# Performance work log

Hardware: AMD Instinct MI355X
Metric: run time of the kernel (lower is better)

Reference implementation:

```python
import math
import jax, jax.numpy as jnp
import numpy as np

EPS = 1e-7
MAX_TANH_ARG = 1.0 - 1e-5

def _norm(x):
    return jnp.sqrt(jnp.sum(x * x, axis=-1, keepdims=True)).clip(EPS)

def logmap0(x):  # Poincare ball, c=1
    n = _norm(x)
    return jnp.arctanh(jnp.clip(n, EPS, MAX_TANH_ARG)) * x / n

def expmap0(v):
    n = _norm(v)
    return jnp.tanh(n) * v / n

def mobius_add(x, y):
    x2 = jnp.sum(x * x, -1, keepdims=True)
    y2 = jnp.sum(y * y, -1, keepdims=True)
    xy = jnp.sum(x * y, -1, keepdims=True)
    num = (1 + 2 * xy + y2) * x + (1 - x2) * y
    den = (1 + 2 * xy + x2 * y2).clip(EPS)
    return num / den

def plin(x, w, b):  # PoincareLinear: tangent-space affine map
    return expmap0(logmap0(x) @ w + b)

def layer_norm(x, eps=1e-6):  # elementwise_affine=False
    m = x.mean(-1, keepdims=True)
    v = ((x - m) ** 2).mean(-1, keepdims=True)
    return (x - m) / jnp.sqrt(v + eps)

def _beta(a, b):
    return math.exp(math.lgamma(a) + math.lgamma(b) - math.lgamma(a + b))

D, H, FF = 1024, 16, 4096
HD = D // H
BETA_N = _beta(D / 2, 0.5)   # beta(n/2, 1/2) for full dim
BETA_H = _beta(HD / 2, 0.5)  # beta(ni/2, 1/2) for head dim


def setup_inputs() -> dict:
    key = jax.random.key(0)
    ks = jax.random.split(key, 20)
    B, S = 4, 1024
    x = expmap0(0.02 * jax.random.normal(ks[0], (B, S, D), jnp.float32))
    t_emb = jax.random.normal(ks[1], (B, 1, D), jnp.float32)
    g = lambda k, sh: 0.02 * jax.random.normal(k, sh, jnp.float32)
    return {
        'x': x, 't_emb': t_emb,
        'w_q': g(ks[2], (D, D)), 'b_q': jnp.zeros((D,), jnp.float32),
        'w_k': g(ks[3], (D, D)), 'b_k': jnp.zeros((D,), jnp.float32),
        'w_v': g(ks[4], (D, D)), 'b_v': jnp.zeros((D,), jnp.float32),
        'w_o': g(ks[5], (D, D)), 'b_o': jnp.zeros((D,), jnp.float32),
        'w_f1': g(ks[6], (D, FF)), 'b_f1': jnp.zeros((FF,), jnp.float32),
        'w_f2': g(ks[7], (FF, D)), 'b_f2': jnp.zeros((D,), jnp.float32),
        'w_ada': g(ks[8], (D, 6 * D)), 'b_ada': jnp.zeros((6 * D,), jnp.float32),
    }


def _to_heads(p):
    # beta-split: logmap0, split per head, scale by beta_ni/beta_n, expmap0
    B, S, _ = p.shape
    t = logmap0(p).reshape(B, S, H, HD) * (BETA_H / BETA_N)
    return expmap0(jnp.transpose(t, (0, 2, 1, 3)))  # [B,H,S,HD]


def _from_heads(ph):
    # beta-concat: logmap0 per head, scale by beta_n/beta_ni, concat, expmap0
    B, _, S, _ = ph.shape
    t = logmap0(ph) * (BETA_N / BETA_H)
    t = jnp.transpose(t, (0, 2, 1, 3)).reshape(B, S, D)
    return expmap0(t)


def reference(x, t_emb, w_q, b_q, w_k, b_k, w_v, b_v, w_o, b_o,
              w_f1, b_f1, w_f2, b_f2, w_ada, b_ada):
    ada = t_emb @ w_ada + b_ada  # [B,1,6D]
    sh_msa, sc_msa, g_msa, sh_mlp, sc_mlp, g_mlp = jnp.split(ada, 6, axis=-1)

    # --- attention block ---
    residual = x
    xn = layer_norm(logmap0(x))
    xm = expmap0(xn * (1 + sc_msa) + sh_msa)

    q = _to_heads(plin(xm, w_q, b_q))
    k = _to_heads(plin(xm, w_k, b_k))
    v = _to_heads(plin(xm, w_v, b_v))

    qt, kt, vt = logmap0(q), logmap0(k), logmap0(v)
    scores = jnp.einsum('bhqd,bhkd->bhqk', qt, kt) / math.sqrt(HD)
    attn = jax.nn.softmax(scores, axis=-1)
    out_h = expmap0(jnp.einsum('bhqk,bhkd->bhqd', attn, vt))  # [B,H,S,HD]

    attn_out = plin(_from_heads(out_h), w_o, b_o)
    attn_t = g_msa * logmap0(attn_out)
    x = mobius_add(residual, expmap0(attn_t))

    # --- FFN block ---
    residual = x
    xn = layer_norm(logmap0(x))
    xm = expmap0(xn * (1 + sc_mlp) + sh_mlp)
    ff = plin(plin(xm, w_f1, b_f1), w_f2, b_f2)
    ff_t = g_mlp * logmap0(ff)
    return mobius_add(residual, expmap0(ff_t))
```

## Files before the change

kernel.cpp:

```cpp
#include <hip/hip_runtime.h>
#include <cmath>


constexpr int kD  = 1024;
constexpr int kH  = 16;
constexpr int kHD = 64;
constexpr int kFF = 4096;
constexpr int kB  = 4;
constexpr int kS  = 1024;
constexpr int kN  = kB * kS;

#define EPSF 1e-7f
#define MTAF (1.0f - 1e-5f)
#define LOG2E 1.4426950408889634f

typedef unsigned int uint32;
typedef unsigned short ushort16;
typedef __attribute__((ext_vector_type(8))) short short8x;
typedef __attribute__((ext_vector_type(4))) float floatx4;

__device__ __forceinline__ ushort16 f2b(float f) {
  union { float f; uint32 u; } x; x.f = f;
  uint32 r = x.u + 0x7fffu + ((x.u >> 16) & 1u);
  return (ushort16)(r >> 16);
}
__device__ __forceinline__ float b2f(ushort16 u) {
  union { uint32 u; float f; } x; x.u = ((uint32)u) << 16;
  return x.f;
}
__device__ __forceinline__ void load_b4(const ushort16* p, float v[4]) {
  uint2 u = *(const uint2*)p;
  v[0] = b2f((ushort16)(u.x & 0xffff)); v[1] = b2f((ushort16)(u.x >> 16));
  v[2] = b2f((ushort16)(u.y & 0xffff)); v[3] = b2f((ushort16)(u.y >> 16));
}
__device__ __forceinline__ void store_b4(ushort16* p, const float v[4]) {
  uint2 u;
  u.x = (uint32)f2b(v[0]) | ((uint32)f2b(v[1]) << 16);
  u.y = (uint32)f2b(v[2]) | ((uint32)f2b(v[3]) << 16);
  *(uint2*)p = u;
}

__device__ __forceinline__ float atanh_clipped(float n) {
  float c = fminf(n, MTAF);
  return 0.5f * logf((1.0f + c) / (1.0f - c));
}
__device__ __forceinline__ float logmap0_scale(float nraw) {
  float n = fmaxf(nraw, EPSF);
  return atanh_clipped(n) / n;
}
__device__ __forceinline__ float expmap0_scale(float nraw) {
  float n = fmaxf(nraw, EPSF);
  return tanhf(n) / n;
}
__device__ __forceinline__ float roundtrip_scale(float nraw) {
  float nu = fmaxf(nraw, EPSF);
  float se = tanhf(nu) / nu;
  float nb = fmaxf(se * nraw, EPSF);
  float sl = atanh_clipped(nb) / nb;
  return sl * se;
}

__device__ __forceinline__ float blockReduceSum256(float v, float* s4) {
#pragma unroll
  for (int o = 32; o > 0; o >>= 1) v += __shfl_xor(v, o);
  int wave = threadIdx.x >> 6;
  if ((threadIdx.x & 63) == 0) s4[wave] = v;
  __syncthreads();
  float r = s4[0] + s4[1] + s4[2] + s4[3];
  __syncthreads();
  return r;
}
__device__ __forceinline__ float redSum16(float v) {
#pragma unroll
  for (int o = 8; o > 0; o >>= 1) v += __shfl_xor(v, o);
  return v;
}

__device__ __forceinline__ void async16(const void* g, void* l) {
  __builtin_amdgcn_global_load_lds(
      (const __attribute__((address_space(1))) uint32*)g,
      (__attribute__((address_space(3))) uint32*)l, 16, 0, 0);
}

__device__ __forceinline__ void transpose_tile(const float* __restrict__ src,
                                               ushort16* __restrict__ dst,
                                               int K, int N, int n0, int k0) {
  __shared__ float T[64][65];
  int tid = threadIdx.x;
#pragma unroll
  for (int p = 0; p < 4; ++p) {
    int idx = p * 1024 + tid * 4;
    int r = idx >> 6, c = idx & 63;
    float4 t = *(const float4*)&src[(size_t)(k0 + r) * N + n0 + c];
    T[r][c] = t.x; T[r][c + 1] = t.y; T[r][c + 2] = t.z; T[r][c + 3] = t.w;
  }
  __syncthreads();
#pragma unroll
  for (int p = 0; p < 4; ++p) {
    int idx = p * 1024 + tid * 4;
    int r = idx >> 6, c = idx & 63;
    float v[4] = {T[c][r], T[c + 1][r], T[c + 2][r], T[c + 3][r]};
    store_b4(&dst[(size_t)(n0 + r) * K + k0 + c], v);
  }
}
__global__ __launch_bounds__(256) void k_transpose_bf16(const float* __restrict__ src,
                                                        ushort16* __restrict__ dst,
                                                        int K, int N) {
  transpose_tile(src, dst, K, N, blockIdx.x * 64, blockIdx.y * 64);
}
__global__ __launch_bounds__(256) void k_transpose4(
    const float* __restrict__ s0, const float* __restrict__ s1,
    const float* __restrict__ s2, const float* __restrict__ s3,
    ushort16* __restrict__ d0, ushort16* __restrict__ d1,
    ushort16* __restrict__ d2, ushort16* __restrict__ d3) {
  const float* src = (blockIdx.z == 0) ? s0 : (blockIdx.z == 1) ? s1
                    : (blockIdx.z == 2) ? s2 : s3;
  ushort16* dst = (blockIdx.z == 0) ? d0 : (blockIdx.z == 1) ? d1
                 : (blockIdx.z == 2) ? d2 : d3;
  transpose_tile(src, dst, kD, kD, blockIdx.x * 64, blockIdx.y * 64);
}

__global__ __launch_bounds__(256) void k_ada(const float* __restrict__ t_emb,
                                             const float* __restrict__ w_ada,
                                             const float* __restrict__ b_ada,
                                             float* __restrict__ ada) {
  __shared__ float te[kD];
  __shared__ float part[4][64];
  int b = blockIdx.y;
  int tid = threadIdx.x;
  {
    float4 t = *(const float4*)&t_emb[b * kD + tid * 4];
    te[tid * 4] = t.x; te[tid * 4 + 1] = t.y; te[tid * 4 + 2] = t.z; te[tid * 4 + 3] = t.w;
  }
  __syncthreads();
  int c = tid & 63, kc = tid >> 6;
  int col = blockIdx.x * 64 + c;
  float acc = 0.f;
#pragma unroll 8
  for (int k = kc * 256; k < kc * 256 + 256; ++k)
    acc += te[k] * w_ada[(size_t)k * (6 * kD) + col];
  part[kc][c] = acc;
  __syncthreads();
  if (tid < 64)
    ada[b * 6 * kD + blockIdx.x * 64 + tid] =
        part[0][tid] + part[1][tid] + part[2][tid] + part[3][tid] +
        b_ada[blockIdx.x * 64 + tid];
}

__global__ __launch_bounds__(256) void k_prenorm(const float* __restrict__ x,
                                                 const float* __restrict__ ada,
                                                 int sh_off, int sc_off,
                                                 ushort16* __restrict__ out) {
  __shared__ float sred[4];
  int tok = blockIdx.x;
  int b = tok >> 10;
  int d4 = threadIdx.x * 4;
  float xv[4];
  *(float4*)xv = *(const float4*)&x[(size_t)tok * kD + d4];
  float ss = xv[0] * xv[0] + xv[1] * xv[1] + xv[2] * xv[2] + xv[3] * xv[3];
  ss = blockReduceSum256(ss, sred);
  float sl = logmap0_scale(sqrtf(ss));
  float sum = 0.f;
#pragma unroll
  for (int i = 0; i < 4; ++i) { xv[i] *= sl; sum += xv[i]; }
  sum = blockReduceSum256(sum, sred);
  float mean = sum * (1.0f / kD);
  float vs = 0.f;
#pragma unroll
  for (int i = 0; i < 4; ++i) { xv[i] -= mean; vs += xv[i] * xv[i]; }
  vs = blockReduceSum256(vs, sred);
  float inv = rsqrtf(vs * (1.0f / kD) + 1e-6f);
  float shv[4], scv[4];
  *(float4*)shv = *(const float4*)&ada[b * 6 * kD + sh_off + d4];
  *(float4*)scv = *(const float4*)&ada[b * 6 * kD + sc_off + d4];
  float uu = 0.f;
#pragma unroll
  for (int i = 0; i < 4; ++i) {
    float u = xv[i] * inv * (1.0f + scv[i]) + shv[i];
    xv[i] = u;
    uu += u * u;
  }
  uu = blockReduceSum256(uu, sred);
  float s = roundtrip_scale(sqrtf(uu));
#pragma unroll
  for (int i = 0; i < 4; ++i) xv[i] *= s;
  store_b4(out + (size_t)tok * kD + d4, xv);
}

template <int OUT_BF16, int KSPLIT>
__global__ __launch_bounds__(256) void k_gemm_bf16(
    const ushort16* __restrict__ A,
    const ushort16* __restrict__ Bt0, const ushort16* __restrict__ Bt1,
    const ushort16* __restrict__ Bt2,
    const float* __restrict__ bias0, const float* __restrict__ bias1,
    const float* __restrict__ bias2,
    void* __restrict__ C0, void* __restrict__ C1, void* __restrict__ C2,
    int M, int N, int K) {
  const ushort16* Bt;
  const float* bias;
  void* C;
  int k_lo, k_hi;
  bool add_bias;
  if (KSPLIT == 1) {
    Bt = (blockIdx.z == 0) ? Bt0 : ((blockIdx.z == 1) ? Bt1 : Bt2);
    bias = (blockIdx.z == 0) ? bias0 : ((blockIdx.z == 1) ? bias1 : bias2);
    C = (blockIdx.z == 0) ? C0 : ((blockIdx.z == 1) ? C1 : C2);
    k_lo = 0; k_hi = K; add_bias = true;
  } else {
    Bt = Bt0; bias = bias0;
    C = (blockIdx.z == 0) ? C0 : C1;
    int kchunk = K / KSPLIT;
    k_lo = blockIdx.z * kchunk; k_hi = k_lo + kchunk;
    add_bias = (blockIdx.z == 0);
  }

  __shared__ __align__(16) ushort16 As[128 * 32];
  __shared__ __align__(16) ushort16 Bs[128 * 32];

  int tid = threadIdx.x;
  int lane = tid & 63;
  int wave = tid >> 6;
  int wm = (wave >> 1) * 64, wn = (wave & 1) * 64;
  int row0 = blockIdx.x * 128, col0 = blockIdx.y * 128;

  int e0 = tid * 8;
  int ar0 = e0 >> 5, ac0 = e0 & 31;
  int e1 = e0 + 2048;
  int ar1 = e1 >> 5, ac1 = e1 & 31;
  const ushort16* Ag = A + (size_t)row0 * K;
  const ushort16* Bg = Bt + (size_t)col0 * K;

  floatx4 acc[4][4];
#pragma unroll
  for (int i = 0; i < 4; ++i)
#pragma unroll
    for (int j = 0; j < 4; ++j) acc[i][j] = (floatx4)0.f;

  for (int k0 = k_lo; k0 < k_hi; k0 += 32) {
    async16(Ag + (size_t)ar0 * K + k0 + ac0, As + e0);
    async16(Ag + (size_t)ar1 * K + k0 + ac1, As + e1);
    async16(Bg + (size_t)ar0 * K + k0 + ac0, Bs + e0);
    async16(Bg + (size_t)ar1 * K + k0 + ac1, Bs + e1);
    __syncthreads();

    short8x a[4], b[4];
#pragma unroll
    for (int i = 0; i < 4; ++i) {
      a[i] = *(const short8x*)&As[(wm + i * 16 + (lane & 15)) * 32 + (lane >> 4) * 8];
      b[i] = *(const short8x*)&Bs[(wn + i * 16 + (lane & 15)) * 32 + (lane >> 4) * 8];
    }
#pragma unroll
    for (int i = 0; i < 4; ++i)
#pragma unroll
      for (int j = 0; j < 4; ++j)
        acc[i][j] = __builtin_amdgcn_mfma_f32_16x16x32_bf16(a[i], b[j], acc[i][j], 0, 0, 0);
    __syncthreads();
  }

  float bv[4];
#pragma unroll
  for (int j = 0; j < 4; ++j)
    bv[j] = add_bias ? bias[col0 + wn + j * 16 + (lane & 15)] : 0.f;
  int rowq = (lane >> 4) * 4;
#pragma unroll
  for (int i = 0; i < 4; ++i) {
    int rbase = row0 + wm + i * 16 + rowq;
#pragma unroll
    for (int j = 0; j < 4; ++j) {
      int c = col0 + wn + j * 16 + (lane & 15);
#pragma unroll
      for (int r = 0; r < 4; ++r) {
        float v = acc[i][j][r] + bv[j];
        if (OUT_BF16)
          ((ushort16*)C)[(size_t)(rbase + r) * N + c] = f2b(v);
        else
          ((float*)C)[(size_t)(rbase + r) * N + c] = v;
      }
    }
  }
}

__global__ __launch_bounds__(256) void k_headsplit_b(const ushort16* __restrict__ q_in,
                                                     ushort16* __restrict__ k_io,
                                                     ushort16* __restrict__ v_io,
                                                     ushort16* __restrict__ qb_out,
                                                     float ratio) {
  __shared__ float sred[4];
  int tok = blockIdx.x;
  int tid = threadIdx.x;
  int d4 = tid * 4;
#pragma unroll
  for (int t = 0; t < 3; ++t) {
    const ushort16* p = (t == 0 ? q_in : (t == 1 ? (const ushort16*)k_io
                                                 : (const ushort16*)v_io)) +
                        (size_t)tok * kD + d4;
    float val[4];
    load_b4(p, val);
    float psq = val[0] * val[0] + val[1] * val[1] + val[2] * val[2] + val[3] * val[3];
    float hsq = redSum16(psq);
    float tot = blockReduceSum256(psq, sred);
    float s1 = roundtrip_scale(sqrtf(tot));
    float c = s1 * ratio;
    float s2 = roundtrip_scale(c * sqrtf(hsq));
    float f = c * s2 * (t == 0 ? (0.125f * LOG2E) : 1.0f);
#pragma unroll
    for (int i = 0; i < 4; ++i) val[i] *= f;
    ushort16* op = (t == 0 ? qb_out : (t == 1 ? k_io : v_io)) + (size_t)tok * kD + d4;
    store_b4(op, val);
    __syncthreads();
  }
}

__global__ __launch_bounds__(256) void k_vtrans_b(const ushort16* __restrict__ v,
                                                  ushort16* __restrict__ vT) {
  __shared__ ushort16 T[64][68];
  int bh = blockIdx.y, b = bh >> 4, h = bh & 15;
  int s0 = blockIdx.x * 64;
  int tid = threadIdx.x;
#pragma unroll
  for (int p = 0; p < 4; ++p) {
    int idx = p * 1024 + tid * 4;
    int r = idx >> 6, d = idx & 63;
    *(uint2*)&T[r][d] = *(const uint2*)&v[(size_t)(b * kS + s0 + r) * kD + h * kHD + d];
  }
  __syncthreads();
#pragma unroll
  for (int p = 0; p < 16; ++p) {
    int idx = p * 256 + tid;
    int d = idx >> 6, c = idx & 63;
    int cp = (c & 32) | ((c & 15) << 1) | ((c >> 4) & 1);
    vT[((size_t)bh * kHD + d) * kS + s0 + cp] = T[c][d];
  }
}

__global__ __launch_bounds__(256) void k_attn_mfma(const ushort16* __restrict__ qb,
                                                   const ushort16* __restrict__ kb,
                                                   const ushort16* __restrict__ vT,
                                                   float* __restrict__ outp,
                                                   float ratio2) {
  __shared__ __align__(16) ushort16 Ks[2 * 128 * 32];
  __shared__ __align__(16) ushort16 Vs[4 * 64 * 32];
  __shared__ __align__(16) ushort16 Ps[4 * 4 * 16 * 40];
  int bh = blockIdx.x, b = bh >> 4, h = bh & 15;
  int q0 = blockIdx.y * 128;
  int tid = threadIdx.x, lane = tid & 63, wave = tid >> 6;
  int c16 = lane & 15, quad = lane >> 4;
  int wq = wave * 32;

  short8x a_q[2][2];
#pragma unroll
  for (int i = 0; i < 2; ++i)
#pragma unroll
    for (int kk = 0; kk < 2; ++kk)
      a_q[i][kk] = *(const short8x*)&qb[(size_t)(b * kS + q0 + wq + i * 16 + c16) * kD +
                                        h * kHD + kk * 32 + quad * 8];

  short8x ones;
#pragma unroll
  for (int j = 0; j < 8; ++j) ones[j] = (short)0x3F80;

  floatx4 o[2][4], ol[2];
#pragma unroll
  for (int i = 0; i < 2; ++i) {
    ol[i] = (floatx4)0.f;
#pragma unroll
    for (int n = 0; n < 4; ++n) o[i][n] = (floatx4)0.f;
  }

  const ushort16* kbase = kb + ((size_t)b * kS) * kD + h * kHD;
  const ushort16* vbase = vT + (size_t)bh * kHD * kS;

  for (int k0 = 0; k0 < kS; k0 += 128) {
#pragma unroll
    for (int t = 0; t < 2; ++t)
#pragma unroll
      for (int cb = 0; cb < 2; ++cb) {
        int e = cb * 2048 + tid * 8;
        async16(kbase + (size_t)(k0 + (e >> 5)) * kD + t * 32 + (e & 31),
                Ks + t * 4096 + e);
      }
#pragma unroll
    for (int t = 0; t < 4; ++t) {
      int e = tid * 8;
      async16(vbase + (size_t)(e >> 5) * kS + k0 + t * 32 + (e & 31),
              Vs + t * 2048 + e);
    }
    __syncthreads();

#pragma unroll
    for (int i = 0; i < 2; ++i) {
      floatx4 s[8];
#pragma unroll
      for (int n = 0; n < 8; ++n) s[n] = (floatx4)0.f;
#pragma unroll
      for (int kkd = 0; kkd < 2; ++kkd)
#pragma unroll
        for (int n = 0; n < 8; ++n) {
          short8x bk = *(const short8x*)&Ks[kkd * 4096 + (n * 16 + c16) * 32 + quad * 8];
          s[n] = __builtin_amdgcn_mfma_f32_16x16x32_bf16(a_q[i][kkd], bk, s[n], 0, 0, 0);
        }

#pragma unroll
      for (int r = 0; r < 4; ++r) {
#pragma unroll
        for (int j = 0; j < 4; ++j) {
          uint32 u0 = (uint32)f2b(exp2f(s[2 * j][r]));
          uint32 u1 = (uint32)f2b(exp2f(s[2 * j + 1][r]));
          *(uint32*)&Ps[(((wave * 4 + j) * 16) + (quad * 4 + r)) * 40 + c16 * 2] =
              u0 | (u1 << 16);
        }
      }

#pragma unroll
      for (int kk = 0; kk < 4; ++kk) {
        short8x ap = *(const short8x*)&Ps[(((wave * 4 + kk) * 16) + c16) * 40 + quad * 8];
#pragma unroll
        for (int n = 0; n < 4; ++n) {
          short8x bv = *(const short8x*)&Vs[kk * 2048 + (n * 16 + c16) * 32 + quad * 8];
          o[i][n] = __builtin_amdgcn_mfma_f32_16x16x32_bf16(ap, bv, o[i][n], 0, 0, 0);
        }
        ol[i] = __builtin_amdgcn_mfma_f32_16x16x32_bf16(ap, ones, ol[i], 0, 0, 0);
      }
    }
    __syncthreads();
  }

#pragma unroll
  for (int i = 0; i < 2; ++i)
#pragma unroll
    for (int r = 0; r < 4; ++r) {
      float invl = 1.0f / ol[i][r];
      float w[4];
      float pssq = 0.f;
#pragma unroll
      for (int n = 0; n < 4; ++n) { w[n] = o[i][n][r] * invl; pssq += w[n] * w[n]; }
      float ssq = redSum16(pssq);
      float coef = roundtrip_scale(sqrtf(ssq)) * ratio2;
      int row = b * kS + q0 + wq + i * 16 + quad * 4 + r;
#pragma unroll
      for (int n = 0; n < 4; ++n)
        outp[(size_t)row * kD + h * kHD + n * 16 + c16] = coef * w[n];
    }
}

template <int WIDTH>
__global__ __launch_bounds__(256) void k_rt_scale_f2b(const float* __restrict__ p,
                                                      ushort16* __restrict__ out) {
  __shared__ float sred[4];
  constexpr int PER = WIDTH / 1024;
  size_t base = (size_t)blockIdx.x * WIDTH;
  float v[PER][4];
  float ss = 0.f;
#pragma unroll
  for (int i = 0; i < PER; ++i) {
    *(float4*)v[i] = *(const float4*)&p[base + i * 1024 + threadIdx.x * 4];
#pragma unroll
    for (int j = 0; j < 4; ++j) ss += v[i][j] * v[i][j];
  }
  ss = blockReduceSum256(ss, sred);
  float s = roundtrip_scale(sqrtf(ss));
#pragma unroll
  for (int i = 0; i < PER; ++i) {
#pragma unroll
    for (int j = 0; j < 4; ++j) v[i][j] *= s;
    store_b4(out + base + i * 1024 + threadIdx.x * 4, v[i]);
  }
}

template <int WIDTH>
__global__ __launch_bounds__(256) void k_rt_scale_b2b(ushort16* __restrict__ p) {
  __shared__ float sred[4];
  constexpr int PER = WIDTH / 1024;
  size_t base = (size_t)blockIdx.x * WIDTH;
  float v[PER][4];
  float ss = 0.f;
#pragma unroll
  for (int i = 0; i < PER; ++i) {
    load_b4(p + base + i * 1024 + threadIdx.x * 4, v[i]);
#pragma unroll
    for (int j = 0; j < 4; ++j) ss += v[i][j] * v[i][j];
  }
  ss = blockReduceSum256(ss, sred);
  float s = roundtrip_scale(sqrtf(ss));
#pragma unroll
  for (int i = 0; i < PER; ++i) {
#pragma unroll
    for (int j = 0; j < 4; ++j) v[i][j] *= s;
    store_b4(p + base + i * 1024 + threadIdx.x * 4, v[i]);
  }
}

__device__ __forceinline__ void mobius_body(float xv[4], float tv[4],
                                            const float* gp, int d4,
                                            float* sred, float outv[4]) {
  float ss = tv[0] * tv[0] + tv[1] * tv[1] + tv[2] * tv[2] + tv[3] * tv[3];
  ss = blockReduceSum256(ss, sred);
  float s5 = roundtrip_scale(sqrtf(ss));
  float gv[4];
  *(float4*)gv = *(const float4*)&gp[d4];
  float at2 = 0.f;
#pragma unroll
  for (int i = 0; i < 4; ++i) {
    float a = gv[i] * s5 * tv[i];
    tv[i] = a;
    at2 += a * a;
  }
  at2 = blockReduceSum256(at2, sred);
  float nyraw = sqrtf(at2);
  float sy = expmap0_scale(nyraw);
  float ynorm = sy * nyraw;
  float y2 = ynorm * ynorm;
  float x2p = 0.f, xyp = 0.f;
#pragma unroll
  for (int i = 0; i < 4; ++i) {
    float y = sy * tv[i];
    tv[i] = y;
    x2p += xv[i] * xv[i];
    xyp += xv[i] * y;
  }
  float x2 = blockReduceSum256(x2p, sred);
  float xy = blockReduceSum256(xyp, sred);
  float cx = 1.0f + 2.0f * xy + y2;
  float cy = 1.0f - x2;
  float den = fmaxf(1.0f + 2.0f * xy + x2 * y2, EPSF);
  float invden = 1.0f / den;
#pragma unroll
  for (int i = 0; i < 4; ++i) outv[i] = (cx * xv[i] + cy * tv[i]) * invden;
}

__global__ __launch_bounds__(256) void k_epilogue2(const float* __restrict__ xres,
                                                   const float* __restrict__ ot0,
                                                   const float* __restrict__ ot1,
                                                   const float* __restrict__ ada,
                                                   int g_off,
                                                   float* __restrict__ out) {
  __shared__ float sred[4];
  int tok = blockIdx.x;
  int b = tok >> 10;
  size_t base = (size_t)tok * kD;
  int d4 = threadIdx.x * 4;
  float xv[4], tv[4], t0[4], t1[4];
  *(float4*)t0 = *(const float4*)&ot0[base + d4];
  *(float4*)t1 = *(const float4*)&ot1[base + d4];
  *(float4*)xv = *(const float4*)&xres[base + d4];
#pragma unroll
  for (int i = 0; i < 4; ++i) tv[i] = t0[i] + t1[i];
  float outv[4];
  mobius_body(xv, tv, ada + b * 6 * kD + g_off, d4, sred, outv);
  *(float4*)&out[base + d4] = *(float4*)outv;
}

__global__ __launch_bounds__(256) void k_epi_pre(const float* __restrict__ xres,
                                                 const float* __restrict__ ot0,
                                                 const float* __restrict__ ot1,
                                                 const float* __restrict__ ada,
                                                 float* __restrict__ xmid_out,
                                                 ushort16* __restrict__ lx2_out) {
  __shared__ float sred[4];
  int tok = blockIdx.x;
  int b = tok >> 10;
  size_t base = (size_t)tok * kD;
  int d4 = threadIdx.x * 4;
  float xv[4], tv[4], t0[4], t1[4];
  *(float4*)t0 = *(const float4*)&ot0[base + d4];
  *(float4*)t1 = *(const float4*)&ot1[base + d4];
  *(float4*)xv = *(const float4*)&xres[base + d4];
#pragma unroll
  for (int i = 0; i < 4; ++i) tv[i] = t0[i] + t1[i];
  float xm[4];
  mobius_body(xv, tv, ada + b * 6 * kD + 2 * kD, d4, sred, xm);
  *(float4*)&xmid_out[base + d4] = *(float4*)xm;

  float ss = xm[0] * xm[0] + xm[1] * xm[1] + xm[2] * xm[2] + xm[3] * xm[3];
  ss = blockReduceSum256(ss, sred);
  float sl = logmap0_scale(sqrtf(ss));
  float sum = 0.f;
#pragma unroll
  for (int i = 0; i < 4; ++i) { xm[i] *= sl; sum += xm[i]; }
  sum = blockReduceSum256(sum, sred);
  float mean = sum * (1.0f / kD);
  float vs = 0.f;
#pragma unroll
  for (int i = 0; i < 4; ++i) { xm[i] -= mean; vs += xm[i] * xm[i]; }
  vs = blockReduceSum256(vs, sred);
  float inv = rsqrtf(vs * (1.0f / kD) + 1e-6f);
  float shv[4], scv[4];
  *(float4*)shv = *(const float4*)&ada[b * 6 * kD + 3 * kD + d4];
  *(float4*)scv = *(const float4*)&ada[b * 6 * kD + 4 * kD + d4];
  float uu = 0.f;
#pragma unroll
  for (int i = 0; i < 4; ++i) {
    float u = xm[i] * inv * (1.0f + scv[i]) + shv[i];
    xm[i] = u;
    uu += u * u;
  }
  uu = blockReduceSum256(uu, sred);
  float s = roundtrip_scale(sqrtf(uu));
#pragma unroll
  for (int i = 0; i < 4; ++i) xm[i] *= s;
  store_b4(lx2_out + base + d4, xm);
}

extern "C" void kernel_launch(void* const* d_in, const int* in_sizes, int n_in,
                              void* d_out, int out_size, void* d_ws, size_t ws_size,
                              hipStream_t stream) {
  const float* x     = (const float*)d_in[0];
  const float* t_emb = (const float*)d_in[1];
  const float* w_q = (const float*)d_in[2];  const float* b_q = (const float*)d_in[3];
  const float* w_k = (const float*)d_in[4];  const float* b_k = (const float*)d_in[5];
  const float* w_v = (const float*)d_in[6];  const float* b_v = (const float*)d_in[7];
  const float* w_o = (const float*)d_in[8];  const float* b_o = (const float*)d_in[9];
  const float* w_f1 = (const float*)d_in[10]; const float* b_f1 = (const float*)d_in[11];
  const float* w_f2 = (const float*)d_in[12]; const float* b_f2 = (const float*)d_in[13];
  const float* w_ada = (const float*)d_in[14]; const float* b_ada = (const float*)d_in[15];
  float* out = (float*)d_out;

  constexpr size_t ND = (size_t)kN * kD;
  constexpr size_t NF = (size_t)kN * kFF;
  constexpr size_t DD = (size_t)kD * kD;

  float* ws   = (float*)d_ws;
  float* ada  = ws;
  float* qt   = ada + 6 * kD * kB;
  float* kt   = qt + ND;
  float* vt   = kt + ND;
  ushort16* qbA = (ushort16*)(vt + ND);
  ushort16* kb  = qbA + ND;
  ushort16* vTb = kb + ND;
  ushort16* actB = vTb + ND;
  ushort16* wqT  = actB + NF;
  ushort16* wkT  = wqT + DD;
  ushort16* wvT  = wkT + DD;
  ushort16* woT  = wvT + DD;
  ushort16* wf1T = woT + DD;
  ushort16* wf2T = wf1T + (size_t)kD * kFF;

  double bn = exp(lgamma(512.0) + lgamma(0.5) - lgamma(512.5));
  double bh = exp(lgamma(32.0) + lgamma(0.5) - lgamma(32.5));
  float R1 = (float)(bh / bn);
  float R2 = (float)(bn / bh);

  k_transpose4<<<dim3(16, 16, 4), 256, 0, stream>>>(w_q, w_k, w_v, w_o,
                                                    wqT, wkT, wvT, woT);
  k_transpose_bf16<<<dim3(64, 16), 256, 0, stream>>>(w_f1, wf1T, kD, kFF);
  k_transpose_bf16<<<dim3(16, 64), 256, 0, stream>>>(w_f2, wf2T, kFF, kD);
  k_ada<<<dim3(6 * kD / 64, kB), 256, 0, stream>>>(t_emb, w_ada, b_ada, ada);
  k_prenorm<<<kN, 256, 0, stream>>>(x, ada, 0 * kD, 1 * kD, qbA);
  k_gemm_bf16<1, 1><<<dim3(kN / 128, kD / 128, 3), 256, 0, stream>>>(
      qbA, wqT, wkT, wvT, b_q, b_k, b_v, kb, vTb, actB, kN, kD, kD);
  k_headsplit_b<<<kN, 256, 0, stream>>>(kb, vTb, actB, qbA, R1);
  k_vtrans_b<<<dim3(kS / 64, kB * kH), 256, 0, stream>>>(actB, kb);
  k_attn_mfma<<<dim3(kB * kH, kS / 128), 256, 0, stream>>>(qbA, vTb, kb, kt, R2);
  k_rt_scale_f2b<kD><<<kN, 256, 0, stream>>>(kt, qbA);
  k_gemm_bf16<0, 2><<<dim3(kN / 128, kD / 128, 2), 256, 0, stream>>>(
      qbA, woT, woT, woT, b_o, b_o, b_o, qt, vt, vt, kN, kD, kD);
  k_epi_pre<<<kN, 256, 0, stream>>>(x, qt, vt, ada, vt, qbA);
  k_gemm_bf16<1, 1><<<dim3(kN / 128, kFF / 128, 1), 256, 0, stream>>>(
      qbA, wf1T, wf1T, wf1T, b_f1, b_f1, b_f1, actB, actB, actB, kN, kFF, kD);
  k_rt_scale_b2b<kFF><<<kN, 256, 0, stream>>>(actB);
  k_gemm_bf16<0, 2><<<dim3(kN / 128, kD / 128, 2), 256, 0, stream>>>(
      actB, wf2T, wf2T, wf2T, b_f2, b_f2, b_f2, qt, kt, kt, kN, kD, kFF);
  k_epilogue2<<<kN, 256, 0, stream>>>(vt, qt, kt, ada, 5 * kD, out);

  (void)in_sizes; (void)n_in; (void)out_size; (void)ws_size;
}
```

Measured before the change: 464.5 us.

## Swizzle LDS tiles, fold row roundtrip scale into GEMM epilogue, narrow intermediates

Applies an XOR swizzle to the shared-memory layout of the GEMM and attention K/V tiles to reduce LDS bank conflicts on the MFMA operand reads. The per-row roundtrip scaling kernels that rewrote whole activations are replaced by a kernel that computes only one scale per row. The GEMM epilogue then multiplies by that scale, which is valid because the scale is per row and commutes with the matmul. The attention output is written directly as bf16, and the second split-K partial is stored as bf16 to cut memory traffic. This adds precision loss on one partial sum and slightly more epilogue work.

```diff
diff --git a/kernel.cpp b/kernel.cpp
--- a/kernel.cpp
+++ b/kernel.cpp
@@ -194,6 +194,7 @@
     const ushort16* __restrict__ Bt2,
     const float* __restrict__ bias0, const float* __restrict__ bias1,
     const float* __restrict__ bias2,
+    const float* __restrict__ rowscale,
     void* __restrict__ C0, void* __restrict__ C1, void* __restrict__ C2,
     int M, int N, int K) {
   const ushort16* Bt;
@@ -224,11 +225,17 @@
   int row0 = blockIdx.x * 128, col0 = blockIdx.y * 128;
 
   int e0 = tid * 8;
-  int ar0 = e0 >> 5, ac0 = e0 & 31;
+  int ar0 = e0 >> 5;
+  int ac0 = ((((e0 >> 3) & 3) ^ ((ar0 >> 1) & 3)) << 3);
   int e1 = e0 + 2048;
-  int ar1 = e1 >> 5, ac1 = e1 & 31;
+  int ar1 = e1 >> 5;
+  int ac1 = ((((e1 >> 3) & 3) ^ ((ar1 >> 1) & 3)) << 3);
   const ushort16* Ag = A + (size_t)row0 * K;
   const ushort16* Bg = Bt + (size_t)col0 * K;
+
+  int c16 = lane & 15, quad = lane >> 4;
+  int sw = (lane >> 1) & 3;
+  int cbp = ((quad ^ sw) << 3);
 
   floatx4 acc[4][4];
 #pragma unroll
@@ -246,8 +253,8 @@
     short8x a[4], b[4];
 #pragma unroll
     for (int i = 0; i < 4; ++i) {
-      a[i] = *(const short8x*)&As[(wm + i * 16 + (lane & 15)) * 32 + (lane >> 4) * 8];
-      b[i] = *(const short8x*)&Bs[(wn + i * 16 + (lane & 15)) * 32 + (lane >> 4) * 8];
+      a[i] = *(const short8x*)&As[(wm + i * 16 + c16) * 32 + cbp];
+      b[i] = *(const short8x*)&Bs[(wn + i * 16 + c16) * 32 + cbp];
     }
 #pragma unroll
     for (int i = 0; i < 4; ++i)
@@ -260,21 +267,28 @@
   float bv[4];
 #pragma unroll
   for (int j = 0; j < 4; ++j)
-    bv[j] = add_bias ? bias[col0 + wn + j * 16 + (lane & 15)] : 0.f;
-  int rowq = (lane >> 4) * 4;
+    bv[j] = add_bias ? bias[col0 + wn + j * 16 + c16] : 0.f;
+  int rowq = quad * 4;
 #pragma unroll
   for (int i = 0; i < 4; ++i) {
     int rbase = row0 + wm + i * 16 + rowq;
+    float rs4[4];
+#pragma unroll
+    for (int r = 0; r < 4; ++r) rs4[r] = rowscale ? rowscale[rbase + r] : 1.0f;
 #pragma unroll
     for (int j = 0; j < 4; ++j) {
-      int c = col0 + wn + j * 16 + (lane & 15);
+      int c = col0 + wn + j * 16 + c16;
 #pragma unroll
       for (int r = 0; r < 4; ++r) {
-        float v = acc[i][j][r] + bv[j];
-        if (OUT_BF16)
+        float v = acc[i][j][r] * rs4[r] + bv[j];
+        if (KSPLIT == 2) {
+          if (blockIdx.z == 0) ((float*)C)[(size_t)(rbase + r) * N + c] = v;
+          else ((ushort16*)C)[(size_t)(rbase + r) * N + c] = f2b(v);
+        } else if (OUT_BF16) {
           ((ushort16*)C)[(size_t)(rbase + r) * N + c] = f2b(v);
-        else
+        } else {
           ((float*)C)[(size_t)(rbase + r) * N + c] = v;
+        }
       }
     }
   }
@@ -333,10 +347,9 @@
   }
 }
 
-__global__ __launch_bounds__(256) void k_attn_mfma(const ushort16* __restrict__ qb,
+__global__ __launch_bounds__(256) void k_attn_mfma(ushort16* __restrict__ qb,
                                                    const ushort16* __restrict__ kb,
                                                    const ushort16* __restrict__ vT,
-                                                   float* __restrict__ outp,
                                                    float ratio2) {
   __shared__ __align__(16) ushort16 Ks[2 * 128 * 32];
   __shared__ __align__(16) ushort16 Vs[4 * 64 * 32];
@@ -345,6 +358,8 @@
   int q0 = blockIdx.y * 128;
   int tid = threadIdx.x, lane = tid & 63, wave = tid >> 6;
   int c16 = lane & 15, quad = lane >> 4;
+  int sw = (lane >> 1) & 3;
+  int cbp = ((quad ^ sw) << 3);
   int wq = wave * 32;
 
   short8x a_q[2][2];
@@ -374,16 +389,18 @@
 #pragma unroll
     for (int t = 0; t < 2; ++t)
 #pragma unroll
-      for (int cb = 0; cb < 2; ++cb) {
-        int e = cb * 2048 + tid * 8;
-        async16(kbase + (size_t)(k0 + (e >> 5)) * kD + t * 32 + (e & 31),
-                Ks + t * 4096 + e);
+      for (int cb2 = 0; cb2 < 2; ++cb2) {
+        int e = cb2 * 2048 + tid * 8;
+        int key = e >> 5;
+        int col = ((((e >> 3) & 3) ^ ((key >> 1) & 3)) << 3);
+        async16(kbase + (size_t)(k0 + key) * kD + t * 32 + col, Ks + t * 4096 + e);
       }
 #pragma unroll
     for (int t = 0; t < 4; ++t) {
       int e = tid * 8;
-      async16(vbase + (size_t)(e >> 5) * kS + k0 + t * 32 + (e & 31),
-              Vs + t * 2048 + e);
+      int dd = e >> 5;
+      int col = ((((e >> 3) & 3) ^ ((dd >> 1) & 3)) << 3);
+      async16(vbase + (size_t)dd * kS + k0 + t * 32 + col, Vs + t * 2048 + e);
     }
     __syncthreads();
 
@@ -396,7 +413,7 @@
       for (int kkd = 0; kkd < 2; ++kkd)
 #pragma unroll
         for (int n = 0; n < 8; ++n) {
-          short8x bk = *(const short8x*)&Ks[kkd * 4096 + (n * 16 + c16) * 32 + quad * 8];
+          short8x bk = *(const short8x*)&Ks[kkd * 4096 + (n * 16 + c16) * 32 + cbp];
           s[n] = __builtin_amdgcn_mfma_f32_16x16x32_bf16(a_q[i][kkd], bk, s[n], 0, 0, 0);
         }
 
@@ -416,7 +433,7 @@
         short8x ap = *(const short8x*)&Ps[(((wave * 4 + kk) * 16) + c16) * 40 + quad * 8];
 #pragma unroll
         for (int n = 0; n < 4; ++n) {
-          short8x bv = *(const short8x*)&Vs[kk * 2048 + (n * 16 + c16) * 32 + quad * 8];
+          short8x bv = *(const short8x*)&Vs[kk * 2048 + (n * 16 + c16) * 32 + cbp];
           o[i][n] = __builtin_amdgcn_mfma_f32_16x16x32_bf16(ap, bv, o[i][n], 0, 0, 0);
         }
         ol[i] = __builtin_amdgcn_mfma_f32_16x16x32_bf16(ap, ones, ol[i], 0, 0, 0);
@@ -439,55 +456,25 @@
       int row = b * kS + q0 + wq + i * 16 + quad * 4 + r;
 #pragma unroll
       for (int n = 0; n < 4; ++n)
-        outp[(size_t)row * kD + h * kHD + n * 16 + c16] = coef * w[n];
+        qb[(size_t)row * kD + h * kHD + n * 16 + c16] = f2b(coef * w[n]);
     }
 }
 
 template <int WIDTH>
-__global__ __launch_bounds__(256) void k_rt_scale_f2b(const float* __restrict__ p,
-                                                      ushort16* __restrict__ out) {
+__global__ __launch_bounds__(256) void k_rowscale(const ushort16* __restrict__ p,
+                                                  float* __restrict__ s) {
   __shared__ float sred[4];
   constexpr int PER = WIDTH / 1024;
   size_t base = (size_t)blockIdx.x * WIDTH;
-  float v[PER][4];
   float ss = 0.f;
 #pragma unroll
   for (int i = 0; i < PER; ++i) {
-    *(float4*)v[i] = *(const float4*)&p[base + i * 1024 + threadIdx.x * 4];
-#pragma unroll
-    for (int j = 0; j < 4; ++j) ss += v[i][j] * v[i][j];
+    float v[4];
+    load_b4(p + base + i * 1024 + threadIdx.x * 4, v);
+    ss += v[0] * v[0] + v[1] * v[1] + v[2] * v[2] + v[3] * v[3];
   }
   ss = blockReduceSum256(ss, sred);
-  float s = roundtrip_scale(sqrtf(ss));
-#pragma unroll
-  for (int i = 0; i < PER; ++i) {
-#pragma unroll
-    for (int j = 0; j < 4; ++j) v[i][j] *= s;
-    store_b4(out + base + i * 1024 + threadIdx.x * 4, v[i]);
-  }
-}
-
-template <int WIDTH>
-__global__ __launch_bounds__(256) void k_rt_scale_b2b(ushort16* __restrict__ p) {
-  __shared__ float sred[4];
-  constexpr int PER = WIDTH / 1024;
-  size_t base = (size_t)blockIdx.x * WIDTH;
-  float v[PER][4];
-  float ss = 0.f;
-#pragma unroll
-  for (int i = 0; i < PER; ++i) {
-    load_b4(p + base + i * 1024 + threadIdx.x * 4, v[i]);
-#pragma unroll
-    for (int j = 0; j < 4; ++j) ss += v[i][j] * v[i][j];
-  }
-  ss = blockReduceSum256(ss, sred);
-  float s = roundtrip_scale(sqrtf(ss));
-#pragma unroll
-  for (int i = 0; i < PER; ++i) {
-#pragma unroll
-    for (int j = 0; j < 4; ++j) v[i][j] *= s;
-    store_b4(p + base + i * 1024 + threadIdx.x * 4, v[i]);
-  }
+  if (threadIdx.x == 0) s[blockIdx.x] = roundtrip_scale(sqrtf(ss));
 }
 
 __device__ __forceinline__ void mobius_body(float xv[4], float tv[4],
@@ -530,7 +517,7 @@
 
 __global__ __launch_bounds__(256) void k_epilogue2(const float* __restrict__ xres,
                                                    const float* __restrict__ ot0,
-                                                   const float* __restrict__ ot1,
+                                                   const ushort16* __restrict__ ot1b,
                                                    const float* __restrict__ ada,
                                                    int g_off,
                                                    float* __restrict__ out) {
@@ -539,12 +526,12 @@
   int b = tok >> 10;
   size_t base = (size_t)tok * kD;
   int d4 = threadIdx.x * 4;
-  float xv[4], tv[4], t0[4], t1[4];
-  *(float4*)t0 = *(const float4*)&ot0[base + d4];
-  *(float4*)t1 = *(const float4*)&ot1[base + d4];
+  float xv[4], tv[4], t1[4];
+  *(float4*)tv = *(const float4*)&ot0[base + d4];
+  load_b4(ot1b + base + d4, t1);
   *(float4*)xv = *(const float4*)&xres[base + d4];
 #pragma unroll
-  for (int i = 0; i < 4; ++i) tv[i] = t0[i] + t1[i];
+  for (int i = 0; i < 4; ++i) tv[i] += t1[i];
   float outv[4];
   mobius_body(xv, tv, ada + b * 6 * kD + g_off, d4, sred, outv);
   *(float4*)&out[base + d4] = *(float4*)outv;
@@ -552,7 +539,7 @@
 
 __global__ __launch_bounds__(256) void k_epi_pre(const float* __restrict__ xres,
                                                  const float* __restrict__ ot0,
-                                                 const float* __restrict__ ot1,
+                                                 const ushort16* __restrict__ ot1b,
                                                  const float* __restrict__ ada,
                                                  float* __restrict__ xmid_out,
                                                  ushort16* __restrict__ lx2_out) {
@@ -561,12 +548,12 @@
   int b = tok >> 10;
   size_t base = (size_t)tok * kD;
   int d4 = threadIdx.x * 4;
-  float xv[4], tv[4], t0[4], t1[4];
-  *(float4*)t0 = *(const float4*)&ot0[base + d4];
-  *(float4*)t1 = *(const float4*)&ot1[base + d4];
+  float xv[4], tv[4], t1[4];
+  *(float4*)tv = *(const float4*)&ot0[base + d4];
+  load_b4(ot1b + base + d4, t1);
   *(float4*)xv = *(const float4*)&xres[base + d4];
 #pragma unroll
-  for (int i = 0; i < 4; ++i) tv[i] = t0[i] + t1[i];
+  for (int i = 0; i < 4; ++i) tv[i] += t1[i];
   float xm[4];
   mobius_body(xv, tv, ada + b * 6 * kD + 2 * kD, d4, sred, xm);
   *(float4*)&xmid_out[base + d4] = *(float4*)xm;
@@ -647,20 +634,20 @@
   k_ada<<<dim3(6 * kD / 64, kB), 256, 0, stream>>>(t_emb, w_ada, b_ada, ada);
   k_prenorm<<<kN, 256, 0, stream>>>(x, ada, 0 * kD, 1 * kD, qbA);
   k_gemm_bf16<1, 1><<<dim3(kN / 128, kD / 128, 3), 256, 0, stream>>>(
-      qbA, wqT, wkT, wvT, b_q, b_k, b_v, kb, vTb, actB, kN, kD, kD);
+      qbA, wqT, wkT, wvT, b_q, b_k, b_v, nullptr, kb, vTb, actB, kN, kD, kD);
   k_headsplit_b<<<kN, 256, 0, stream>>>(kb, vTb, actB, qbA, R1);
   k_vtrans_b<<<dim3(kS / 64, kB * kH), 256, 0, stream>>>(actB, kb);
-  k_attn_mfma<<<dim3(kB * kH, kS / 128), 256, 0, stream>>>(qbA, vTb, kb, kt, R2);
-  k_rt_scale_f2b<kD><<<kN, 256, 0, stream>>>(kt, qbA);
+  k_attn_mfma<<<dim3(kB * kH, kS / 128), 256, 0, stream>>>(qbA, vTb, kb, R2);
+  k_rowscale<kD><<<kN, 256, 0, stream>>>(qbA, kt);
   k_gemm_bf16<0, 2><<<dim3(kN / 128, kD / 128, 2), 256, 0, stream>>>(
-      qbA, woT, woT, woT, b_o, b_o, b_o, qt, vt, vt, kN, kD, kD);
-  k_epi_pre<<<kN, 256, 0, stream>>>(x, qt, vt, ada, vt, qbA);
+      qbA, woT, woT, woT, b_o, b_o, b_o, kt, qt, kb, nullptr, kN, kD, kD);
+  k_epi_pre<<<kN, 256, 0, stream>>>(x, qt, kb, ada, vt, qbA);
   k_gemm_bf16<1, 1><<<dim3(kN / 128, kFF / 128, 1), 256, 0, stream>>>(
-      qbA, wf1T, wf1T, wf1T, b_f1, b_f1, b_f1, actB, actB, actB, kN, kFF, kD);
-  k_rt_scale_b2b<kFF><<<kN, 256, 0, stream>>>(actB);
+      qbA, wf1T, wf1T, wf1T, b_f1, b_f1, b_f1, nullptr, actB, actB, actB, kN, kFF, kD);
+  k_rowscale<kFF><<<kN, 256, 0, stream>>>(actB, kt);
   k_gemm_bf16<0, 2><<<dim3(kN / 128, kD / 128, 2), 256, 0, stream>>>(
-      actB, wf2T, wf2T, wf2T, b_f2, b_f2, b_f2, qt, kt, kt, kN, kD, kFF);
-  k_epilogue2<<<kN, 256, 0, stream>>>(vt, qt, kt, ada, 5 * kD, out);
+      actB, wf2T, wf2T, wf2T, b_f2, b_f2, b_f2, kt, qt, kb, nullptr, kN, kD, kFF);
+  k_epilogue2<<<kN, 256, 0, stream>>>(vt, qt, kb, ada, 5 * kD, out);
 
   (void)in_sizes; (void)n_in; (void)out_size; (void)ws_size;
 }
```

Measured after the change: 451.8 us. 2.7% less time.
